# Performance work log

Hardware: AMD Instinct MI355X
Metric: run time of the kernel (lower is better)

Reference implementation:

```python
import jax, jax.numpy as jnp
import numpy as np
import math

B, L, HID = 2, 1024, 1536
NH, HD = 24, 64
DSSM = NH * HD            # 1536 (expand = 1)
QKV = 3 * DSSM
DCONV = 2
EPS = 1e-6


def _silu(u):
    return u * jax.nn.sigmoid(u)


def setup_inputs() -> dict:
    key = jax.random.key(0)
    ks = jax.random.split(key, 10)
    x = jax.random.normal(ks[0], (B, L, HID), dtype=jnp.float32)
    w_qkv = jax.random.normal(ks[1], (QKV, HID), dtype=jnp.float32) / math.sqrt(HID)
    conv_w = jax.random.normal(ks[2], (QKV, DCONV), dtype=jnp.float32) * 0.5  # depthwise causal conv, k=2
    w_dt = jax.random.normal(ks[3], (NH, HID), dtype=jnp.float32) * 0.02
    # dt_bias init exactly as in the torch module
    dt = jnp.exp(jax.random.uniform(ks[4], (NH,)) * (math.log(0.1) - math.log(0.001)) + math.log(0.001))
    dt = jnp.clip(dt, 1e-4, None)
    dt_bias = dt + jnp.log(-jnp.expm1(-dt))
    a_log = jnp.log(jax.random.uniform(ks[5], (NH,), minval=1.0, maxval=16.0))
    D = jnp.ones((NH, HD), dtype=jnp.float32)
    w_z = jax.random.normal(ks[6], (DSSM, HID), dtype=jnp.float32) / math.sqrt(HID)
    b_z = jnp.zeros((DSSM,), dtype=jnp.float32)
    rms_w = jnp.ones((DSSM,), dtype=jnp.float32)
    w_o = jax.random.normal(ks[7], (HID, DSSM), dtype=jnp.float32) / math.sqrt(DSSM)
    return dict(x=x, w_qkv=w_qkv, conv_w=conv_w, w_dt=w_dt, dt_bias=dt_bias,
                a_log=a_log, D=D, w_z=w_z, b_z=b_z, rms_w=rms_w, w_o=w_o)


def reference(x, w_qkv, conv_w, w_dt, dt_bias, a_log, D, w_z, b_z, rms_w, w_o):
    # qkv projection  [B,L,3*DSSM]
    qkv = jnp.einsum('blh,qh->blq', x, w_qkv)
    # depthwise causal conv1d (kernel size 2, padding k-1, trimmed to L)
    prev = jnp.pad(qkv, ((0, 0), (1, 0), (0, 0)))[:, :L]
    qkv = _silu(prev * conv_w[:, 0] + qkv * conv_w[:, 1])
    q, k, v = jnp.split(qkv, 3, axis=-1)
    q = q.reshape(B, L, NH, HD)
    k = k.reshape(B, L, NH, HD)
    v = v.reshape(B, L, NH, HD)
    # dt discretization: softplus(dt_proj(x) + dt_bias)   [B,L,NH]
    dt = jax.nn.softplus(jnp.einsum('blh,nh->bln', x, w_dt) + dt_bias)
    A = -jnp.exp(a_log)              # [NH], negative
    dA = dt * A                      # [B,L,NH]
    cs = jnp.transpose(jnp.cumsum(dA, axis=1), (0, 2, 1))   # [B,NH,L]
    diff = cs[:, :, :, None] - cs[:, :, None, :]            # [B,NH,L,L], <=0 on causal part
    causal = jnp.tril(jnp.ones((L, L), dtype=bool))
    decay = jnp.exp(jnp.where(causal, diff, -jnp.inf))      # segment-sum decay matrix
    # quadratic SSD (attention) form of the selective scan
    scores = jnp.einsum('bihd,bjhd->bhij', q, k) * decay
    scores = scores * jnp.transpose(dt, (0, 2, 1))[:, :, None, :]  # dt_j on keys (B-discretization)
    y = jnp.einsum('bhij,bjhd->bihd', scores, v)
    y = y + v * D                    # D skip connection
    y = y.reshape(B, L, DSSM)
    # z gate + RMSNorm + output projection
    z = jnp.einsum('blh,dh->bld', x, w_z) + b_z
    y = y * _silu(z)
    y = y * jax.lax.rsqrt(jnp.mean(y * y, axis=-1, keepdims=True) + EPS) * rms_w
    return jnp.einsum('bld,hd->blh', y, w_o)
```

## Files before the change

kernel.cpp:

```cpp
#include <hip/hip_runtime.h>
#include <hip/hip_bf16.h>
#include <math.h>

#define B_ 2
#define L_ 1024
#define HID_ 1536
#define NH_ 24
#define HD_ 64
#define DSSM_ 1536
#define QKV_ 4608
#define M_ 2048

typedef __attribute__((ext_vector_type(8))) short short8;
typedef __attribute__((ext_vector_type(4))) short short4e;
typedef __attribute__((ext_vector_type(4))) float floatx4;

__device__ __forceinline__ void gload_lds16(const short* g, short* l)
{
    __builtin_amdgcn_global_load_lds(
        (const __attribute__((address_space(1))) void*)g,
        (__attribute__((address_space(3))) void*)l,
        16, 0, 0);
}

__device__ __forceinline__ float bfs2f(short s)
{
    unsigned u = ((unsigned)(unsigned short)s) << 16;
    float f; __builtin_memcpy(&f, &u, 4); return f;
}
__device__ __forceinline__ short f2bfs(float f)
{
    __hip_bfloat16 h = __float2bfloat16(f);
    short s; __builtin_memcpy(&s, &h, 2); return s;
}

__device__ const int kIt[30] = {0,1,2,3,4,5, 6,6, 7,7, 8,8, 9,9, 10,10, 11,11,
                                12,12,12, 13,13,13, 14,14,14, 15,15,15};
__device__ const int kS[30]  = {0,0,0,0,0,0, 0,1, 0,1, 0,1, 0,1, 0,1, 0,1,
                                0,1,2, 0,1,2, 0,1,2, 0,1,2};

#define CN0 (M_ * HID_)
#define CN1 (QKV_ * HID_)
#define CN2 (DSSM_ * HID_)
#define CN3 (HID_ * DSSM_)
__global__ void cast_w_kernel(
    const float* __restrict__ wq,
    const float* __restrict__ wz, const float* __restrict__ wo,
    __hip_bfloat16* __restrict__ wcat,
    __hip_bfloat16* __restrict__ wob)
{
    int i = (blockIdx.x * 256 + threadIdx.x) * 4;
    const float* src; __hip_bfloat16* dst; int off;
    if (i < CN1)             { src = wq; dst = wcat;       off = i; }
    else if (i < CN1 + CN2)  { src = wz; dst = wcat + CN1; off = i - CN1; }
    else                     { src = wo; dst = wob;        off = i - CN1 - CN2; }
    float4 f = *reinterpret_cast<const float4*>(src + off);
    dst[off]     = __float2bfloat16(f.x);
    dst[off + 1] = __float2bfloat16(f.y);
    dst[off + 2] = __float2bfloat16(f.z);
    dst[off + 3] = __float2bfloat16(f.w);
}

#define MFMA_ __builtin_amdgcn_mfma_f32_16x16x32_bf16
#define BAR_() __builtin_amdgcn_s_barrier()
#define SCHED_ __builtin_amdgcn_sched_barrier(0)

#define CSTR 200

__global__ __launch_bounds__(256, 2) void gemm_qkvz_128(
    const __hip_bfloat16* __restrict__ A,
    const __hip_bfloat16* __restrict__ Bm,
    __hip_bfloat16* __restrict__ qkv_out,
    float* __restrict__ z_out,
    const float* __restrict__ b_z)
{
    extern __shared__ short lds[];
    const int K  = HID_;
    const int NT = K / 64;
    const int tid   = threadIdx.x;
    const int lane  = tid & 63;
    const int wave  = tid >> 6;
    const int col16 = lane & 15;
    const int quad  = lane >> 4;
    const int wm = wave >> 1;
    const int wn = wave & 1;
    const int rowblk = blockIdx.y * 128;
    const int colblk = blockIdx.x * 192;

    const short* Ap = reinterpret_cast<const short*>(A);
    const short* Bp = reinterpret_cast<const short*>(Bm);

    const int o  = tid * 16;
    const int s  = o ^ (((o >> 7) & 7) << 4);
    const int sr = s >> 7;
    const int sc = (s & 127) >> 1;

    const int mask = (col16 & 7) << 4;
    const int e0 = ((quad * 16)      ^ mask) >> 1;
    const int e1 = ((64 + quad * 16) ^ mask) >> 1;
    const int arow = (wm * 64 + col16) * 64;
    const int brow = (wn * 96 + col16) * 64;

    floatx4 acc[4][6] = {};

    auto STAGE_ALL = [&](int c, int t) {
        const short* ga = Ap + (size_t)(rowblk + sr) * K + t * 64 + sc;
        short* da = &lds[c * 8192 + tid * 8];
#pragma unroll
        for (int u = 0; u < 4; ++u)
            gload_lds16(ga + (size_t)(u * 32) * K, da + u * 2048);
        const short* gb = Bp + (size_t)(colblk + sr) * K + t * 64 + sc;
        short* db = &lds[16384 + c * 12288 + tid * 8];
#pragma unroll
        for (int u = 0; u < 6; ++u)
            gload_lds16(gb + (size_t)(u * 32) * K, db + u * 2048);
    };

    STAGE_ALL(0, 0);
    asm volatile("s_waitcnt vmcnt(0)" ::: "memory");
    SCHED_;
    BAR_();

    for (int t = 0; t < NT; ++t) {
        const int cur = t & 1;
        if (t + 1 < NT) STAGE_ALL(cur ^ 1, t + 1);

        const int Ab = cur * 8192;
        const int Bb = 16384 + cur * 12288;
        short8 af0[4], af1[4], bf0[6], bf1[6];
#pragma unroll
        for (int m = 0; m < 4; ++m) {
            af0[m] = *reinterpret_cast<const short8*>(&lds[Ab + arow + m * 1024 + e0]);
            af1[m] = *reinterpret_cast<const short8*>(&lds[Ab + arow + m * 1024 + e1]);
        }
#pragma unroll
        for (int n = 0; n < 6; ++n) {
            bf0[n] = *reinterpret_cast<const short8*>(&lds[Bb + brow + n * 1024 + e0]);
            bf1[n] = *reinterpret_cast<const short8*>(&lds[Bb + brow + n * 1024 + e1]);
        }
        asm volatile("s_waitcnt lgkmcnt(0)" ::: "memory");
        SCHED_;

        __builtin_amdgcn_s_setprio(1);
#pragma unroll
        for (int m = 0; m < 4; ++m)
#pragma unroll
            for (int n = 0; n < 6; ++n) {
                acc[m][n] = MFMA_(af0[m], bf0[n], acc[m][n], 0, 0, 0);
                acc[m][n] = MFMA_(af1[m], bf1[n], acc[m][n], 0, 0, 0);
            }
        __builtin_amdgcn_s_setprio(0);

        asm volatile("s_waitcnt vmcnt(0)" ::: "memory");
        SCHED_;
        BAR_();
    }

    if (blockIdx.x < 24) {
        const int rb = wm * 64 + quad * 4;
        const int cb = wn * 96 + col16;
#pragma unroll
        for (int m = 0; m < 4; ++m)
#pragma unroll
            for (int n = 0; n < 6; ++n)
#pragma unroll
                for (int r = 0; r < 4; ++r)
                    lds[(rb + m * 16 + r) * CSTR + cb + n * 16] =
                        f2bfs(acc[m][n][r]);
        __syncthreads();
        const int row = tid >> 1;
        const int seg = tid & 1;
        const short* srcp = &lds[row * CSTR + seg * 96];
        short* dstp = reinterpret_cast<short*>(qkv_out)
                    + (size_t)(rowblk + row) * QKV_ + colblk + seg * 96;
#pragma unroll
        for (int j = 0; j < 12; ++j)
            *reinterpret_cast<short8*>(dstp + j * 8) =
                *reinterpret_cast<const short8*>(srcp + j * 8);
    } else {
        const int row0  = rowblk + wm * 64;
        const int col0g = colblk + wn * 96 - QKV_;
#pragma unroll
        for (int m = 0; m < 4; ++m)
#pragma unroll
            for (int n = 0; n < 6; ++n)
#pragma unroll
                for (int r = 0; r < 4; ++r) {
                    int row = row0 + m * 16 + quad * 4 + r;
                    int col = col0g + n * 16 + col16;
                    z_out[(size_t)row * DSSM_ + col] = acc[m][n][r] + b_z[col];
                }
    }
}

template<int OUTMODE>
__global__ __launch_bounds__(256) void gemm_nt(
    const __hip_bfloat16* __restrict__ A,
    const __hip_bfloat16* __restrict__ Bm,
    void* __restrict__ Cv,
    const float* __restrict__ bias,
    int M, int N, int K)
{
    const int lane  = threadIdx.x & 63;
    const int wave  = threadIdx.x >> 6;
    const int col16 = lane & 15;
    const int quad  = lane >> 4;
    const int wr    = wave >> 1;
    const int wc    = wave & 1;
    const int rowblk = blockIdx.y * 128;
    const int colblk = blockIdx.x * 128;

    const short* Ap = reinterpret_cast<const short*>(A);
    const short* Bp = reinterpret_cast<const short*>(Bm);

    __shared__ alignas(16) short As[128 * 32];
    __shared__ alignas(16) short Bs[128 * 32];

    const int srow = lane >> 2;
    const int scol = (lane & 3) * 8;

    floatx4 acc[4][4] = {};

    for (int k0 = 0; k0 < K; k0 += 32) {
#pragma unroll
        for (int s2 = 0; s2 < 2; ++s2) {
            const int seg = wave * 2 + s2;
            gload_lds16(Ap + (size_t)(rowblk + seg * 16 + srow) * K + k0 + scol,
                        &As[seg * 512]);
            gload_lds16(Bp + (size_t)(colblk + seg * 16 + srow) * K + k0 + scol,
                        &Bs[seg * 512]);
        }
        __syncthreads();

        short8 af[4], bf[4];
#pragma unroll
        for (int t = 0; t < 4; ++t) {
            af[t] = *reinterpret_cast<const short8*>(
                &As[(wr * 64 + t * 16 + col16) * 32 + quad * 8]);
            bf[t] = *reinterpret_cast<const short8*>(
                &Bs[(wc * 64 + t * 16 + col16) * 32 + quad * 8]);
        }
#pragma unroll
        for (int mt = 0; mt < 4; ++mt)
#pragma unroll
            for (int nt = 0; nt < 4; ++nt)
                acc[mt][nt] = __builtin_amdgcn_mfma_f32_16x16x32_bf16(
                    af[mt], bf[nt], acc[mt][nt], 0, 0, 0);
        __syncthreads();
    }

    const int row0 = rowblk + wr * 64;
    const int col0 = colblk + wc * 64;
#pragma unroll
    for (int mt = 0; mt < 4; ++mt) {
#pragma unroll
        for (int nt = 0; nt < 4; ++nt) {
#pragma unroll
            for (int r = 0; r < 4; ++r) {
                int row = row0 + mt * 16 + quad * 4 + r;
                int col = col0 + nt * 16 + col16;
                float v = acc[mt][nt][r];
                if (OUTMODE == 1) v += bias[col];
                if (OUTMODE == 2)
                    ((__hip_bfloat16*)Cv)[(size_t)row * N + col] = __float2bfloat16(v);
                else
                    ((float*)Cv)[(size_t)row * N + col] = v;
            }
        }
    }
}

__global__ void conv_silu_kernel(
    const __hip_bfloat16* __restrict__ raw,
    const float* __restrict__ conv_w,
    __hip_bfloat16* __restrict__ q,
    __hip_bfloat16* __restrict__ k,
    __hip_bfloat16* __restrict__ v)
{
    int idx8 = blockIdx.x * 256 + threadIdx.x;
    int c8 = (idx8 % (QKV_ / 8)) * 8;
    int ml = idx8 / (QKV_ / 8);
    int l  = ml % L_;
    int b  = ml / L_;

    const short* base = reinterpret_cast<const short*>(raw) + (size_t)ml * QKV_ + c8;
    short8 curv = *reinterpret_cast<const short8*>(base);
    short8 prevv = {};
    if (l > 0) prevv = *reinterpret_cast<const short8*>(base - QKV_);

    float4 w0 = *reinterpret_cast<const float4*>(conv_w + c8 * 2);
    float4 w1 = *reinterpret_cast<const float4*>(conv_w + c8 * 2 + 4);
    float4 w2 = *reinterpret_cast<const float4*>(conv_w + c8 * 2 + 8);
    float4 w3 = *reinterpret_cast<const float4*>(conv_w + c8 * 2 + 12);
    const float wa[16] = {w0.x, w0.y, w0.z, w0.w, w1.x, w1.y, w1.z, w1.w,
                          w2.x, w2.y, w2.z, w2.w, w3.x, w3.y, w3.z, w3.w};

    short8 outv;
#pragma unroll
    for (int j = 0; j < 8; ++j) {
        float u = bfs2f(prevv[j]) * wa[2 * j] + bfs2f(curv[j]) * wa[2 * j + 1];
        u = fmaxf(u, -80.f);
        outv[j] = f2bfs(u / (1.f + __expf(-u)));
    }

    int part = c8 / DSSM_;
    int cc   = c8 % DSSM_;
    int nh   = cc >> 6;
    int d    = cc & 63;
    __hip_bfloat16* dst = (part == 0) ? q : ((part == 1) ? k : v);
    *reinterpret_cast<short8*>(
        reinterpret_cast<short*>(dst) + (((size_t)b * NH_ + nh) * L_ + l) * HD_ + d)
        = outv;
}

__global__ __launch_bounds__(256) void dtproj_kernel(
    const float* __restrict__ x,
    const float* __restrict__ w_dt,
    const float* __restrict__ dt_bias,
    const float* __restrict__ a_log,
    float* __restrict__ dt,
    float* __restrict__ dA,
    __hip_bfloat16* __restrict__ xb)
{
    const int tid  = threadIdx.x;
    const int wave = tid >> 6;
    const int lane = tid & 63;
    const int m0   = blockIdx.x * 8 + wave * 2;

    float4 xa[2][6];
#pragma unroll
    for (int rr = 0; rr < 2; ++rr)
#pragma unroll
        for (int j = 0; j < 6; ++j)
            xa[rr][j] = *reinterpret_cast<const float4*>(
                x + (size_t)(m0 + rr) * HID_ + lane * 4 + j * 256);

    short* xbp = reinterpret_cast<short*>(xb);
#pragma unroll
    for (int rr = 0; rr < 2; ++rr)
#pragma unroll
        for (int j = 0; j < 6; ++j) {
            short4e ov;
            ov[0] = f2bfs(xa[rr][j].x); ov[1] = f2bfs(xa[rr][j].y);
            ov[2] = f2bfs(xa[rr][j].z); ov[3] = f2bfs(xa[rr][j].w);
            *reinterpret_cast<short4e*>(
                xbp + (size_t)(m0 + rr) * HID_ + lane * 4 + j * 256) = ov;
        }

    float acc0[NH_], acc1[NH_];
#pragma unroll
    for (int n = 0; n < NH_; ++n) {
        float s0 = 0.f, s1 = 0.f;
#pragma unroll
        for (int j = 0; j < 6; ++j) {
            float4 w = *reinterpret_cast<const float4*>(
                w_dt + (size_t)n * HID_ + lane * 4 + j * 256);
            s0 += xa[0][j].x * w.x + xa[0][j].y * w.y
                + xa[0][j].z * w.z + xa[0][j].w * w.w;
            s1 += xa[1][j].x * w.x + xa[1][j].y * w.y
                + xa[1][j].z * w.z + xa[1][j].w * w.w;
        }
        acc0[n] = s0;
        acc1[n] = s1;
    }

#pragma unroll
    for (int off = 32; off; off >>= 1) {
#pragma unroll
        for (int n = 0; n < NH_; ++n) {
            acc0[n] += __shfl_xor(acc0[n], off, 64);
            acc1[n] += __shfl_xor(acc1[n], off, 64);
        }
    }

    if (lane < NH_) {
        const int n = lane;
        float bias = dt_bias[n];
        float Aval = -__expf(a_log[n]);
        float v0 = acc0[n] + bias;
        float v1 = acc1[n] + bias;
        v0 = (v0 > 20.f) ? v0 : log1pf(__expf(v0));
        v1 = (v1 > 20.f) ? v1 : log1pf(__expf(v1));
        int b0 = m0 / L_, l0 = m0 % L_;
        size_t o0 = ((size_t)b0 * NH_ + n) * L_ + l0;
        dt[o0]     = v0;
        dA[o0]     = v0 * Aval;
        dt[o0 + 1] = v1;
        dA[o0 + 1] = v1 * Aval;
    }
}

__global__ void cumsum_kernel(const float* __restrict__ dA, float* __restrict__ cs)
{
    int bnh  = blockIdx.x;
    int lane = threadIdx.x;
    const float* src = dA + (size_t)bnh * L_;
    float* dst       = cs + (size_t)bnh * L_;

    float loc[16];
    float run = 0.f;
#pragma unroll
    for (int t = 0; t < 16; ++t) { run += src[lane * 16 + t]; loc[t] = run; }
    float tot = run;
    float sc = tot;
#pragma unroll
    for (int off = 1; off < 64; off <<= 1) {
        float o = __shfl_up(sc, off, 64);
        if (lane >= off) sc += o;
    }
    float offset = sc - tot;
#pragma unroll
    for (int t = 0; t < 16; ++t) dst[lane * 16 + t] = loc[t] + offset;
}

__global__ __launch_bounds__(256) void vdt_transpose_kernel(
    const __hip_bfloat16* __restrict__ v,
    const float* __restrict__ dt,
    __hip_bfloat16* __restrict__ vt)
{
    const int lt0 = blockIdx.x * 64;
    const int bnh = blockIdx.z * NH_ + blockIdx.y;
    const int tid = threadIdx.x;

    __shared__ short T[64][72];

    {
        int row = tid >> 2;
        int cc  = (tid & 3) * 16;
        const short* sp = reinterpret_cast<const short*>(v)
                        + ((size_t)bnh * L_ + lt0 + row) * HD_ + cc;
        float dtr = dt[(size_t)bnh * L_ + lt0 + row];
        short8 a = *reinterpret_cast<const short8*>(sp);
        short8 b = *reinterpret_cast<const short8*>(sp + 8);
#pragma unroll
        for (int j = 0; j < 8; ++j) {
            T[row][cc + j]     = f2bfs(bfs2f(a[j]) * dtr);
            T[row][cc + 8 + j] = f2bfs(bfs2f(b[j]) * dtr);
        }
    }
    __syncthreads();
    {
        int d  = tid >> 2;
        int lc = (tid & 3) * 16;
        short8 o0, o1;
#pragma unroll
        for (int j = 0; j < 8; ++j) {
            o0[j] = T[lc + j][d];
            o1[j] = T[lc + 8 + j][d];
        }
        short* dst = reinterpret_cast<short*>(vt)
                   + ((size_t)bnh * HD_ + d) * L_ + lt0 + lc;
        *reinterpret_cast<short8*>(dst)     = o0;
        *reinterpret_cast<short8*>(dst + 8) = o1;
    }
}

__global__ __launch_bounds__(256) void attn_kernel(
    const __hip_bfloat16* __restrict__ q,
    const __hip_bfloat16* __restrict__ k,
    const __hip_bfloat16* __restrict__ vt,
    const float* __restrict__ cs,
    float* __restrict__ p0,
    float* __restrict__ p1,
    float* __restrict__ p2)
{
    const int bid  = blockIdx.x;
    const int xcd  = bid & 7;
    const int tq   = bid >> 3;
    const int g    = (tq / 30) * 8 + xcd;
    const int pidx = tq % 30;
    const int it   = kIt[pidx];
    const int sl   = kS[pidx];
    const int b    = g / NH_;
    const int nh   = g % NH_;
    const int tid  = threadIdx.x;
    const int lane = tid & 63;
    const int wave = tid >> 6;
    const int col  = lane & 15;
    const int quad = lane >> 4;
    const int bnh  = b * NH_ + nh;
    const int iw0  = it * 64 + wave * 16;

    float* pout = (sl == 0) ? p0 : ((sl == 1) ? p1 : p2);

    const short* qp  = reinterpret_cast<const short*>(q);
    const short* kp  = reinterpret_cast<const short*>(k);
    const short* vtp = reinterpret_cast<const short*>(vt);

    __shared__ alignas(16) short Ks[4096];
    __shared__ alignas(16) short Ps[4 * 16 * 72];
    __shared__ float Cj[384];

    const int jbase = sl * 384;
    const int jlim  = min(384, L_ - jbase);
    if (tid < (jlim >> 2))
        *reinterpret_cast<float4*>(&Cj[tid * 4]) =
            *reinterpret_cast<const float4*>(cs + (size_t)bnh * L_ + jbase + tid * 4);

    const short* qrow = qp + ((size_t)bnh * L_ + iw0 + col) * HD_;
    short8 aq0 = *reinterpret_cast<const short8*>(qrow + quad * 8);
    short8 aq1 = *reinterpret_cast<const short8*>(qrow + 32 + quad * 8);

    float csr[4];
#pragma unroll
    for (int r = 0; r < 4; ++r)
        csr[r] = cs[(size_t)bnh * L_ + iw0 + quad * 4 + r];

    auto STAGE_K = [&](int jt2) {
        const short* gk = kp + ((size_t)bnh * L_ + jt2 * 64 + wave * 16 + (lane >> 2)) * HD_
                        + (lane & 3) * 8;
        gload_lds16(gk,      &Ks[wave * 512 + lane * 8]);
        gload_lds16(gk + 32, &Ks[2048 + wave * 512 + lane * 8]);
    };

    const int jt_beg = sl * 6;
    const int jt_end = min(sl * 6 + 5, it);

    STAGE_K(jt_beg);

    floatx4 accO[4] = {};

    for (int jt = jt_beg; jt <= jt_end; ++jt) {
        const int j0 = jt * 64;

        asm volatile("s_waitcnt vmcnt(0)" ::: "memory");
        SCHED_;
        __syncthreads();

        short8 bv[2][4];
#pragma unroll
        for (int c = 0; c < 2; ++c) {
            if (j0 + c * 32 <= iw0 + 15) {
#pragma unroll
                for (int nt = 0; nt < 4; ++nt)
                    bv[c][nt] = *reinterpret_cast<const short8*>(
                        vtp + ((size_t)bnh * HD_ + nt * 16 + col) * L_
                            + j0 + c * 32 + quad * 8);
            }
        }

#pragma unroll
        for (int s = 0; s < 4; ++s) {
            int jsub = j0 + s * 16;
            if (jsub <= iw0 + 15) {
                short8 bk0 = *reinterpret_cast<const short8*>(
                    &Ks[(s * 16 + col) * 32 + quad * 8]);
                short8 bk1 = *reinterpret_cast<const short8*>(
                    &Ks[2048 + (s * 16 + col) * 32 + quad * 8]);
                floatx4 sc = {};
                sc = __builtin_amdgcn_mfma_f32_16x16x32_bf16(aq0, bk0, sc, 0, 0, 0);
                sc = __builtin_amdgcn_mfma_f32_16x16x32_bf16(aq1, bk1, sc, 0, 0, 0);
                int j = jsub + col;
                float csj = Cj[j - jbase];
#pragma unroll
                for (int r = 0; r < 4; ++r) {
                    int i = iw0 + quad * 4 + r;
                    float e = (j <= i) ? __expf(csr[r] - csj) : 0.f;
                    Ps[wave * 1152 + (quad * 4 + r) * 72 + s * 16 + col] =
                        f2bfs(sc[r] * e);
                }
            } else if (j0 + (s >> 1) * 32 <= iw0 + 15) {
#pragma unroll
                for (int r = 0; r < 4; ++r)
                    Ps[wave * 1152 + (quad * 4 + r) * 72 + s * 16 + col] = 0;
            }
        }

#pragma unroll
        for (int c = 0; c < 2; ++c) {
            if (j0 + c * 32 > iw0 + 15) continue;
            short8 pa = *reinterpret_cast<const short8*>(
                &Ps[wave * 1152 + col * 72 + c * 32 + quad * 8]);
#pragma unroll
            for (int nt = 0; nt < 4; ++nt)
                accO[nt] = __builtin_amdgcn_mfma_f32_16x16x32_bf16(
                    pa, bv[c][nt], accO[nt], 0, 0, 0);
        }

        __syncthreads();
        if (jt < jt_end) STAGE_K(jt + 1);
    }

#pragma unroll
    for (int nt = 0; nt < 4; ++nt) {
#pragma unroll
        for (int r = 0; r < 4; ++r) {
            int i  = iw0 + quad * 4 + r;
            int dv = nt * 16 + col;
            pout[((size_t)b * L_ + i) * DSSM_ + nh * HD_ + dv] = accO[nt][r];
        }
    }
}

__global__ __launch_bounds__(256) void gate_rms_kernel(
    const float* __restrict__ p0,
    const float* __restrict__ p1,
    const float* __restrict__ p2,
    const float* __restrict__ z,
    const __hip_bfloat16* __restrict__ v,
    const float* __restrict__ Dm,
    const float* __restrict__ rms_w,
    __hip_bfloat16* __restrict__ yn)
{
    int m   = blockIdx.x;
    int b   = m / L_;
    int l   = m % L_;
    int tid = threadIdx.x;
    size_t base = (size_t)m * DSSM_;
    const bool has1 = (l >= 384);
    const bool has2 = (l >= 768);

    floatx4 acc4[2] = {};
    float ss = 0.f;
#pragma unroll
    for (int t = 0; t < 2; ++t) {
        int i4 = t * 256 + tid;
        if (i4 < DSSM_ / 4) {
            int c  = i4 * 4;
            int nh = c >> 6, d = c & 63;
            floatx4 p = *reinterpret_cast<const floatx4*>(p0 + base + c);
            if (has1) p += *reinterpret_cast<const floatx4*>(p1 + base + c);
            if (has2) p += *reinterpret_cast<const floatx4*>(p2 + base + c);
            floatx4 dm = *reinterpret_cast<const floatx4*>(Dm + c);
            floatx4 zz = *reinterpret_cast<const floatx4*>(z + base + c);
            short4e vv = *reinterpret_cast<const short4e*>(
                reinterpret_cast<const short*>(v)
                + (((size_t)b * NH_ + nh) * L_ + l) * HD_ + d);
            floatx4 g;
#pragma unroll
            for (int j = 0; j < 4; ++j) {
                float yv = p[j] + bfs2f(vv[j]) * dm[j];
                float zv = fmaxf(zz[j], -80.f);
                float gv = yv * (zv / (1.f + __expf(-zv)));
                ss += gv * gv;
                g[j] = gv;
            }
            acc4[t] = g;
        }
    }
#pragma unroll
    for (int off = 32; off; off >>= 1) ss += __shfl_xor(ss, off, 64);
    __shared__ float red[4];
    if ((tid & 63) == 0) red[tid >> 6] = ss;
    __syncthreads();
    ss = red[0] + red[1] + red[2] + red[3];
    float r = rsqrtf(ss / (float)DSSM_ + 1e-6f);
#pragma unroll
    for (int t = 0; t < 2; ++t) {
        int i4 = t * 256 + tid;
        if (i4 < DSSM_ / 4) {
            int c = i4 * 4;
            floatx4 rw = *reinterpret_cast<const floatx4*>(rms_w + c);
            short4e o;
#pragma unroll
            for (int j = 0; j < 4; ++j)
                o[j] = f2bfs(acc4[t][j] * r * rw[j]);
            *reinterpret_cast<short4e*>(
                reinterpret_cast<short*>(yn) + base + c) = o;
        }
    }
}

extern "C" void kernel_launch(void* const* d_in, const int* in_sizes, int n_in,
                              void* d_out, int out_size, void* d_ws, size_t ws_size,
                              hipStream_t stream)
{
    const float* x       = (const float*)d_in[0];
    const float* w_qkv   = (const float*)d_in[1];
    const float* conv_w  = (const float*)d_in[2];
    const float* w_dt    = (const float*)d_in[3];
    const float* dt_bias = (const float*)d_in[4];
    const float* a_log   = (const float*)d_in[5];
    const float* Dm      = (const float*)d_in[6];
    const float* w_z     = (const float*)d_in[7];
    const float* b_z     = (const float*)d_in[8];
    const float* rms_w   = (const float*)d_in[9];
    const float* w_o     = (const float*)d_in[10];
    float* out = (float*)d_out;

    char* ws = (char*)d_ws;

    __hip_bfloat16* xb    = (__hip_bfloat16*)(ws);
    __hip_bfloat16* wob   = (__hip_bfloat16*)(ws + 6291456);
    float*          zbuf  = (float*)(ws + 11010048);
    __hip_bfloat16* wcat  = (__hip_bfloat16*)(ws + 23592960);
    __hip_bfloat16* qkvb  = (__hip_bfloat16*)(ws + 42467328);
    __hip_bfloat16* qb    = (__hip_bfloat16*)(ws + 61341696);
    __hip_bfloat16* kb    = (__hip_bfloat16*)(ws + 67633152);
    __hip_bfloat16* vb    = (__hip_bfloat16*)(ws + 73924608);
    float* dt   = (float*)(ws + 80216064);
    float* dA   = (float*)(ws + 80412672);
    float* cs   = (float*)(ws + 80609280);
    __hip_bfloat16* vtb = (__hip_bfloat16*)(ws);
    __hip_bfloat16* yn  = (__hip_bfloat16*)(ws);
    float* p0 = (float*)(ws + 23592960);
    float* p1 = (float*)(ws + 36175872);
    float* p2 = (float*)(ws + 48758784);

    static bool attr_set = false;
    if (!attr_set) {
        (void)hipFuncSetAttribute(reinterpret_cast<const void*>(gemm_qkvz_128),
                                  hipFuncAttributeMaxDynamicSharedMemorySize,
                                  81920);
        attr_set = true;
    }

    cast_w_kernel<<<(CN1 + CN2 + CN3) / 1024, 256, 0, stream>>>(
        w_qkv, w_z, w_o, wcat, wob);

    dtproj_kernel<<<M_ / 8, 256, 0, stream>>>(
        x, w_dt, dt_bias, a_log, dt, dA, xb);

    cumsum_kernel<<<B_ * NH_, 64, 0, stream>>>(dA, cs);

    gemm_qkvz_128<<<dim3((QKV_ + DSSM_) / 192, M_ / 128), 256, 81920, stream>>>(
        xb, wcat, qkvb, zbuf, b_z);

    conv_silu_kernel<<<(B_ * L_ * QKV_ / 8) / 256, 256, 0, stream>>>(
        qkvb, conv_w, qb, kb, vb);

    vdt_transpose_kernel<<<dim3(L_ / 64, NH_, B_), 256, 0, stream>>>(vb, dt, vtb);

    attn_kernel<<<1440, 256, 0, stream>>>(
        qb, kb, vtb, cs, p0, p1, p2);

    gate_rms_kernel<<<M_, 256, 0, stream>>>(p0, p1, p2, zbuf, vb, Dm, rms_w, yn);

    gemm_nt<0><<<dim3(HID_ / 128, M_ / 128), 256, 0, stream>>>(
        yn, wob, (void*)out, nullptr, M_, HID_, DSSM_);
}
```

Before: 273.4 us.

## Process two 64-row query tiles per attention block to reuse staged K and V

Each attention block now covers 128 query rows, split into two 64-row halves that per wave share the same staged K tile and V fragments. The key-range split is recomputed for the new tiling, and the grid is halved from 1440 to 720 blocks. This amortises K staging, V loads and the cumsum fetch over twice the work. In exchange it doubles accumulator registers and P shared memory, and there are fewer blocks to fill the GPU.

```diff
diff --git a/kernel.cpp b/kernel.cpp
--- a/kernel.cpp
+++ b/kernel.cpp
@@ -34,10 +34,9 @@
     short s; __builtin_memcpy(&s, &h, 2); return s;
 }
 
-__device__ const int kIt[30] = {0,1,2,3,4,5, 6,6, 7,7, 8,8, 9,9, 10,10, 11,11,
-                                12,12,12, 13,13,13, 14,14,14, 15,15,15};
-__device__ const int kS[30]  = {0,0,0,0,0,0, 0,1, 0,1, 0,1, 0,1, 0,1, 0,1,
-                                0,1,2, 0,1,2, 0,1,2, 0,1,2};
+__device__ const int pIt[15] = {0,1,2,3,3,4,4,5,5,6,6,6,7,7,7};
+__device__ const int pJ0[15] = {0,0,0,0,6,0,6,0,6,0,6,12,0,6,12};
+__device__ const int pSl[15] = {0,0,0,0,1,0,1,0,1,0,1,2,0,1,2};
 
 #define CN0 (M_ * HID_)
 #define CN1 (QKV_ * HID_)
@@ -467,10 +466,11 @@
     const int bid  = blockIdx.x;
     const int xcd  = bid & 7;
     const int tq   = bid >> 3;
-    const int g    = (tq / 30) * 8 + xcd;
-    const int pidx = tq % 30;
-    const int it   = kIt[pidx];
-    const int sl   = kS[pidx];
+    const int g    = (tq / 15) * 8 + xcd;
+    const int pidx = tq % 15;
+    const int it   = pIt[pidx];
+    const int sl   = pSl[pidx];
+    const int jt_beg = pJ0[pidx];
     const int b    = g / NH_;
     const int nh   = g % NH_;
     const int tid  = threadIdx.x;
@@ -479,7 +479,8 @@
     const int col  = lane & 15;
     const int quad = lane >> 4;
     const int bnh  = b * NH_ + nh;
-    const int iw0  = it * 64 + wave * 16;
+    const int iw0  = it * 128 + wave * 16;
+    const int iw1  = iw0 + 64;
 
     float* pout = (sl == 0) ? p0 : ((sl == 1) ? p1 : p2);
 
@@ -488,23 +489,28 @@
     const short* vtp = reinterpret_cast<const short*>(vt);
 
     __shared__ alignas(16) short Ks[4096];
-    __shared__ alignas(16) short Ps[4 * 16 * 72];
+    __shared__ alignas(16) short Ps[4 * 2 * 16 * 72];
     __shared__ float Cj[384];
 
-    const int jbase = sl * 384;
+    const int jbase = jt_beg * 64;
     const int jlim  = min(384, L_ - jbase);
     if (tid < (jlim >> 2))
         *reinterpret_cast<float4*>(&Cj[tid * 4]) =
             *reinterpret_cast<const float4*>(cs + (size_t)bnh * L_ + jbase + tid * 4);
 
-    const short* qrow = qp + ((size_t)bnh * L_ + iw0 + col) * HD_;
-    short8 aq0 = *reinterpret_cast<const short8*>(qrow + quad * 8);
-    short8 aq1 = *reinterpret_cast<const short8*>(qrow + 32 + quad * 8);
-
-    float csr[4];
-#pragma unroll
-    for (int r = 0; r < 4; ++r)
-        csr[r] = cs[(size_t)bnh * L_ + iw0 + quad * 4 + r];
+    const short* qrow0 = qp + ((size_t)bnh * L_ + iw0 + col) * HD_;
+    const short* qrow1 = qp + ((size_t)bnh * L_ + iw1 + col) * HD_;
+    short8 aq0_0 = *reinterpret_cast<const short8*>(qrow0 + quad * 8);
+    short8 aq0_1 = *reinterpret_cast<const short8*>(qrow0 + 32 + quad * 8);
+    short8 aq1_0 = *reinterpret_cast<const short8*>(qrow1 + quad * 8);
+    short8 aq1_1 = *reinterpret_cast<const short8*>(qrow1 + 32 + quad * 8);
+
+    float csr0[4], csr1[4];
+#pragma unroll
+    for (int r = 0; r < 4; ++r) {
+        csr0[r] = cs[(size_t)bnh * L_ + iw0 + quad * 4 + r];
+        csr1[r] = cs[(size_t)bnh * L_ + iw1 + quad * 4 + r];
+    }
 
     auto STAGE_K = [&](int jt2) {
         const short* gk = kp + ((size_t)bnh * L_ + jt2 * 64 + wave * 16 + (lane >> 2)) * HD_
@@ -513,12 +519,12 @@
         gload_lds16(gk + 32, &Ks[2048 + wave * 512 + lane * 8]);
     };
 
-    const int jt_beg = sl * 6;
-    const int jt_end = min(sl * 6 + 5, it);
+    const int jt_end = min(jt_beg + 5, 2 * it + 1);
 
     STAGE_K(jt_beg);
 
-    floatx4 accO[4] = {};
+    floatx4 accO0[4] = {};
+    floatx4 accO1[4] = {};
 
     for (int jt = jt_beg; jt <= jt_end; ++jt) {
         const int j0 = jt * 64;
@@ -530,7 +536,7 @@
         short8 bv[2][4];
 #pragma unroll
         for (int c = 0; c < 2; ++c) {
-            if (j0 + c * 32 <= iw0 + 15) {
+            if (j0 + c * 32 <= iw1 + 15) {
 #pragma unroll
                 for (int nt = 0; nt < 4; ++nt)
                     bv[c][nt] = *reinterpret_cast<const short8*>(
@@ -542,39 +548,66 @@
 #pragma unroll
         for (int s = 0; s < 4; ++s) {
             int jsub = j0 + s * 16;
+            short8 bk0 = *reinterpret_cast<const short8*>(
+                &Ks[(s * 16 + col) * 32 + quad * 8]);
+            short8 bk1 = *reinterpret_cast<const short8*>(
+                &Ks[2048 + (s * 16 + col) * 32 + quad * 8]);
+            int j = jsub + col;
+            float csj = Cj[j - jbase];
+
             if (jsub <= iw0 + 15) {
-                short8 bk0 = *reinterpret_cast<const short8*>(
-                    &Ks[(s * 16 + col) * 32 + quad * 8]);
-                short8 bk1 = *reinterpret_cast<const short8*>(
-                    &Ks[2048 + (s * 16 + col) * 32 + quad * 8]);
                 floatx4 sc = {};
-                sc = __builtin_amdgcn_mfma_f32_16x16x32_bf16(aq0, bk0, sc, 0, 0, 0);
-                sc = __builtin_amdgcn_mfma_f32_16x16x32_bf16(aq1, bk1, sc, 0, 0, 0);
-                int j = jsub + col;
-                float csj = Cj[j - jbase];
+                sc = __builtin_amdgcn_mfma_f32_16x16x32_bf16(aq0_0, bk0, sc, 0, 0, 0);
+                sc = __builtin_amdgcn_mfma_f32_16x16x32_bf16(aq0_1, bk1, sc, 0, 0, 0);
 #pragma unroll
                 for (int r = 0; r < 4; ++r) {
                     int i = iw0 + quad * 4 + r;
-                    float e = (j <= i) ? __expf(csr[r] - csj) : 0.f;
-                    Ps[wave * 1152 + (quad * 4 + r) * 72 + s * 16 + col] =
+                    float e = (j <= i) ? __expf(csr0[r] - csj) : 0.f;
+                    Ps[wave * 2304 + (quad * 4 + r) * 72 + s * 16 + col] =
                         f2bfs(sc[r] * e);
                 }
             } else if (j0 + (s >> 1) * 32 <= iw0 + 15) {
 #pragma unroll
                 for (int r = 0; r < 4; ++r)
-                    Ps[wave * 1152 + (quad * 4 + r) * 72 + s * 16 + col] = 0;
+                    Ps[wave * 2304 + (quad * 4 + r) * 72 + s * 16 + col] = 0;
             }
+
+            if (jsub <= iw1 + 15) {
+                floatx4 sc = {};
+                sc = __builtin_amdgcn_mfma_f32_16x16x32_bf16(aq1_0, bk0, sc, 0, 0, 0);
+                sc = __builtin_amdgcn_mfma_f32_16x16x32_bf16(aq1_1, bk1, sc, 0, 0, 0);
+#pragma unroll
+                for (int r = 0; r < 4; ++r) {
+                    int i = iw1 + quad * 4 + r;
+                    float e = (j <= i) ? __expf(csr1[r] - csj) : 0.f;
+                    Ps[wave * 2304 + 1152 + (quad * 4 + r) * 72 + s * 16 + col] =
+                        f2bfs(sc[r] * e);
+                }
+            } else if (j0 + (s >> 1) * 32 <= iw1 + 15) {
+#pragma unroll
+                for (int r = 0; r < 4; ++r)
+                    Ps[wave * 2304 + 1152 + (quad * 4 + r) * 72 + s * 16 + col] = 0;
+            }
         }
 
 #pragma unroll
         for (int c = 0; c < 2; ++c) {
-            if (j0 + c * 32 > iw0 + 15) continue;
-            short8 pa = *reinterpret_cast<const short8*>(
-                &Ps[wave * 1152 + col * 72 + c * 32 + quad * 8]);
-#pragma unroll
-            for (int nt = 0; nt < 4; ++nt)
-                accO[nt] = __builtin_amdgcn_mfma_f32_16x16x32_bf16(
-                    pa, bv[c][nt], accO[nt], 0, 0, 0);
+            if (j0 + c * 32 <= iw0 + 15) {
+                short8 pa = *reinterpret_cast<const short8*>(
+                    &Ps[wave * 2304 + col * 72 + c * 32 + quad * 8]);
+#pragma unroll
+                for (int nt = 0; nt < 4; ++nt)
+                    accO0[nt] = __builtin_amdgcn_mfma_f32_16x16x32_bf16(
+                        pa, bv[c][nt], accO0[nt], 0, 0, 0);
+            }
+            if (j0 + c * 32 <= iw1 + 15) {
+                short8 pa = *reinterpret_cast<const short8*>(
+                    &Ps[wave * 2304 + 1152 + col * 72 + c * 32 + quad * 8]);
+#pragma unroll
+                for (int nt = 0; nt < 4; ++nt)
+                    accO1[nt] = __builtin_amdgcn_mfma_f32_16x16x32_bf16(
+                        pa, bv[c][nt], accO1[nt], 0, 0, 0);
+            }
         }
 
         __syncthreads();
@@ -585,9 +618,11 @@
     for (int nt = 0; nt < 4; ++nt) {
 #pragma unroll
         for (int r = 0; r < 4; ++r) {
-            int i  = iw0 + quad * 4 + r;
             int dv = nt * 16 + col;
-            pout[((size_t)b * L_ + i) * DSSM_ + nh * HD_ + dv] = accO[nt][r];
+            int i0 = iw0 + quad * 4 + r;
+            int i1 = iw1 + quad * 4 + r;
+            pout[((size_t)b * L_ + i0) * DSSM_ + nh * HD_ + dv] = accO0[nt][r];
+            pout[((size_t)b * L_ + i1) * DSSM_ + nh * HD_ + dv] = accO1[nt][r];
         }
     }
 }
@@ -721,7 +756,7 @@
 
     vdt_transpose_kernel<<<dim3(L_ / 64, NH_, B_), 256, 0, stream>>>(vb, dt, vtb);
 
-    attn_kernel<<<1440, 256, 0, stream>>>(
+    attn_kernel<<<720, 256, 0, stream>>>(
         qb, kb, vtb, cs, p0, p1, p2);
 
     gate_rms_kernel<<<M_, 256, 0, stream>>>(p0, p1, p2, zbuf, vb, Dm, rms_w, yn);
```

Result: faster. 261.8 us (-4.2%).
